# Optimization experiments

Measured on AMD Instinct MI355X. Metric: run time of the kernel, lower is better.

## Reference

```python
import jax, jax.numpy as jnp
import numpy as np

G, N_PER, P_EDGE = 128, 20, 0.2
INPUT_DIM, HIDDEN, OUT_DIM = 32, 64, 10


def _build_structures():
    rng = np.random.default_rng(0)
    n, g = N_PER, G
    A = rng.random((g, n, n)) < P_EDGE
    A = np.triu(A, 1)
    A = A | A.transpose(0, 2, 1)  # symmetric, zero diag
    gi, uu, vv = np.nonzero(A)
    edge_index = np.stack([uu + gi * n, vv + gi * n]).astype(np.int64)
    batch = np.repeat(np.arange(g), n).astype(np.int64)
    # ---- 2-sets ----
    iu, ju = np.triu_indices(n, 1)
    P2 = len(iu)
    M2 = np.zeros((n, n), np.int64)
    M2[iu, ju] = np.arange(P2); M2[ju, iu] = np.arange(P2)
    gu2 = (np.arange(g)[:, None] * n + iu[None]).ravel().astype(np.int64)
    gv2 = (np.arange(g)[:, None] * n + ju[None]).ravel().astype(np.int64)
    iso2 = A[:, iu, ju].astype(np.float32).reshape(-1, 1)
    w = np.arange(n)
    # branch A: (u,v) -> (v,w) if adj[v,w] & w!=u & adj[u,w]; branch B symmetric
    condA = A[:, ju, :] & A[:, iu, :] & (w[None, None, :] != iu[None, :, None])
    condB = A[:, iu, :] & A[:, ju, :] & (w[None, None, :] != ju[None, :, None])
    ga_, ia_, wa_ = np.nonzero(condA)
    gb_, ib_, wb_ = np.nonzero(condB)
    src2 = np.concatenate([ia_ + ga_ * P2, ib_ + gb_ * P2])
    dst2 = np.concatenate([M2[ju[ia_], wa_] + ga_ * P2, M2[iu[ib_], wb_] + gb_ * P2])
    two_edges = np.stack([src2, dst2]).astype(np.int64)
    two_batch = np.repeat(np.arange(g), P2).astype(np.int64)
    # ---- 3-sets ----
    trips = np.array([(a, b, c) for a in range(n) for b in range(a + 1, n) for c in range(b + 1, n)], np.int64)
    a, b, c = trips[:, 0], trips[:, 1], trips[:, 2]
    P3 = len(trips)
    M3 = np.zeros((n, n, n), np.int64)
    M3[a, b, c] = np.arange(P3)
    ga3 = (np.arange(g)[:, None] * n + a[None]).ravel().astype(np.int64)
    gb3 = (np.arange(g)[:, None] * n + b[None]).ravel().astype(np.int64)
    gc3 = (np.arange(g)[:, None] * n + c[None]).ravel().astype(np.int64)
    ec = A[:, a, b].astype(np.int64) + A[:, b, c].astype(np.int64) + A[:, a, c].astype(np.int64)
    iso3 = np.eye(4, dtype=np.float32)[ec.reshape(-1)]
    notin = (w[None] != a[:, None]) & (w[None] != b[:, None]) & (w[None] != c[:, None])  # [P3,n]
    srcs, dsts = [], []
    # branches: replace c (keep a,b), replace b (keep a,c), replace a (keep b,c)
    for k0, k1, nbr in ((a, b, c), (a, c, b), (b, c, a)):
        cond = A[:, nbr, :] & notin[None]
        gg_, ii_, dd_ = np.nonzero(cond)
        tri = np.sort(np.stack([k0[ii_], k1[ii_], dd_], 1), 1)
        srcs.append(ii_ + gg_ * P3)
        dsts.append(M3[tri[:, 0], tri[:, 1], tri[:, 2]] + gg_ * P3)
    three_edges = np.stack([np.concatenate(srcs), np.concatenate(dsts)]).astype(np.int64)
    three_batch = np.repeat(np.arange(g), P3).astype(np.int64)
    x = rng.standard_normal((g * n, INPUT_DIM)).astype(np.float32)
    return (x, edge_index, batch, gu2, gv2, iso2, two_edges, two_batch,
            ga3, gb3, gc3, iso3, three_edges, three_batch)


def setup_inputs() -> dict:
    (x, edge_index, batch, gu2, gv2, iso2, two_edges, two_batch,
     ga3, gb3, gc3, iso3, three_edges, three_batch) = _build_structures()
    rw = np.random.default_rng(1)
    def W(o, i):
        return jnp.asarray((rw.standard_normal((o, i)) * 0.1).astype(np.float32))
    H = HIDDEN
    return dict(
        x=jnp.asarray(x), edge_index=jnp.asarray(edge_index), batch=jnp.asarray(batch),
        gu2=jnp.asarray(gu2), gv2=jnp.asarray(gv2), iso2=jnp.asarray(iso2),
        two_edges=jnp.asarray(two_edges), two_batch=jnp.asarray(two_batch),
        ga3=jnp.asarray(ga3), gb3=jnp.asarray(gb3), gc3=jnp.asarray(gc3),
        iso3=jnp.asarray(iso3), three_edges=jnp.asarray(three_edges),
        three_batch=jnp.asarray(three_batch),
        g1W1_0=W(H, INPUT_DIM), g1W2_0=W(H, INPUT_DIM),
        g1W1_1=W(H, H), g1W2_1=W(H, H), g1W1_2=W(H, H), g1W2_2=W(H, H),
        g2W1_0=W(H, 2 * H + 1), g2W2_0=W(H, 2 * H + 1), g2W1_1=W(H, H), g2W2_1=W(H, H),
        g3W1_0=W(H, 3 * H + 4), g3W2_0=W(H, 3 * H + 4), g3W1_1=W(H, H), g3W2_1=W(H, H),
        cW1=W(H, 3 * H), cb1=jnp.zeros((H,), jnp.float32),
        cW2=W(OUT_DIM, H), cb2=jnp.zeros((OUT_DIM,), jnp.float32),
    )


def _layer(h, W1, W2, src, dst, num):
    # f(s) = relu(h W1^T + scatter_add(h W2^T gathered at src, dst))
    msg = (h @ W2.T)[src]  # project-then-gather; same math as gather-then-project
    nb = jax.ops.segment_sum(msg, dst, num_segments=num)
    return jax.nn.relu(h @ W1.T + nb)


def reference(x, edge_index, batch, gu2, gv2, iso2, two_edges, two_batch,
              ga3, gb3, gc3, iso3, three_edges, three_batch,
              g1W1_0, g1W2_0, g1W1_1, g1W2_1, g1W1_2, g1W2_2,
              g2W1_0, g2W2_0, g2W1_1, g2W2_1,
              g3W1_0, g3W2_0, g3W1_1, g3W2_1,
              cW1, cb1, cW2, cb2):
    N = x.shape[0]
    h = x
    for W1, W2 in ((g1W1_0, g1W2_0), (g1W1_1, g1W2_1), (g1W1_2, g1W2_2)):
        h = _layer(h, W1, W2, edge_index[0], edge_index[1], N)
    emb1 = jax.ops.segment_sum(h, batch, num_segments=G)
    h2 = jnp.concatenate([h[gu2], h[gv2], iso2], axis=1)
    n2 = h2.shape[0]
    for W1, W2 in ((g2W1_0, g2W2_0), (g2W1_1, g2W2_1)):
        h2 = _layer(h2, W1, W2, two_edges[0], two_edges[1], n2)
    emb2 = jax.ops.segment_sum(h2, two_batch, num_segments=G)
    h3 = jnp.concatenate([h[ga3], h[gb3], h[gc3], iso3], axis=1)
    n3 = h3.shape[0]
    for W1, W2 in ((g3W1_0, g3W2_0), (g3W1_1, g3W2_1)):
        h3 = _layer(h3, W1, W2, three_edges[0], three_edges[1], n3)
    emb3 = jax.ops.segment_sum(h3, three_batch, num_segments=G)
    comb = jnp.concatenate([emb1, emb2, emb3], axis=1)
    hid = jax.nn.relu(comb @ cW1.T + cb1)  # dropout is identity in eval mode
    return hid @ cW2.T + cb2
```

## Files before the change

kernel.cpp:

```cpp
#include <hip/hip_runtime.h>
#include <hip/hip_bf16.h>

#define HID 64
#define MROWS 1140
#define PAD1 20
#define PAD2 40
#define PAD3 60

typedef __hip_bfloat16  bf16;
typedef __hip_bfloat162 bf162;
typedef unsigned short  u16;
typedef __attribute__((ext_vector_type(8))) short bf8v;
typedef __attribute__((ext_vector_type(4))) float f4v;
typedef __attribute__((ext_vector_type(4))) unsigned int u4v;
__device__ __forceinline__ float bl(bf16 h) { return __bfloat162float(h); }

__global__ void zero_k(int* p, int n) {
    int i = blockIdx.x * 256 + threadIdx.x;
    if (i < n) p[i] = 0;
}

__global__ void fillp_k(const int* e1, int E1, int* c1, u16* s1, int p1, int P1_,
                        const int* e2, int E2, int* c2, u16* s2, int p2, int P2_,
                        const int* e3, int E3, int* c3, u16* s3, int p3, int P3_,
                        int nb1, int nb2) {
    int b = blockIdx.x;
    const int* edges; int E; int* cur; u16* csrc; int pad; int P; int lb;
    if (b < nb1)            { edges = e1; E = E1; cur = c1; csrc = s1; pad = p1; P = P1_; lb = b; }
    else if (b < nb1 + nb2) { edges = e2; E = E2; cur = c2; csrc = s2; pad = p2; P = P2_; lb = b - nb1; }
    else                    { edges = e3; E = E3; cur = c3; csrc = s3; pad = p3; P = P3_; lb = b - nb1 - nb2; }
    int e = lb * 256 + threadIdx.x;
    if (e >= E) return;
    int d = edges[E + e];
    int slot = atomicAdd(&cur[d], 1);
    if (slot < pad) csrc[(size_t)d * pad + slot] = (u16)(edges[e] % P);
}

__global__ __launch_bounds__(256)
void level1_k(const float* __restrict__ x,
              const int* __restrict__ cnt1, const u16* __restrict__ csrc1,
              const float* __restrict__ W10, const float* __restrict__ W20,
              const float* __restrict__ W11, const float* __restrict__ W21,
              const float* __restrict__ W12, const float* __restrict__ W22,
              float* __restrict__ hout, float* __restrict__ comb, int nper) {
    __shared__ float hbuf[20][64];
    __shared__ float mbuf[20][64];
    __shared__ float wl1[64 * 64];
    __shared__ float wl2[64 * 64];
    int g = blockIdx.x, t = threadIdx.x;
    int wv = t >> 6, lane = t & 63;
    int base = g * nper;
    for (int i = t; i < 20 * 32; i += 256)
        hbuf[i >> 5][i & 31] = x[(size_t)base * 32 + i];
    const float* W1s[3] = {W10, W11, W12};
    const float* W2s[3] = {W20, W21, W22};
#pragma unroll 1
    for (int l = 0; l < 3; ++l) {
        int K = (l == 0) ? 32 : 64;
        const float* W1 = W1s[l];
        const float* W2 = W2s[l];
        __syncthreads();
        for (int i = t; i < K * 64; i += 256) {
            int k = i >> 6, col = i & 63;
            wl1[i] = W1[col * K + k];
            wl2[i] = W2[col * K + k];
        }
        __syncthreads();
        float accz[5], accm[5];
#pragma unroll
        for (int ri = 0; ri < 5; ++ri) {
            int r = wv + ri * 4;
            float az = 0.f, am = 0.f;
            for (int k = 0; k < K; ++k) {
                float hv = hbuf[r][k];
                az = fmaf(hv, wl1[k * 64 + lane], az);
                am = fmaf(hv, wl2[k * 64 + lane], am);
            }
            accz[ri] = az; accm[ri] = am;
        }
        __syncthreads();
#pragma unroll
        for (int ri = 0; ri < 5; ++ri)
            mbuf[wv + ri * 4][lane] = accm[ri];
        __syncthreads();
#pragma unroll
        for (int ri = 0; ri < 5; ++ri) {
            int r = wv + ri * 4;
            float acc = accz[ri];
            int cnt = cnt1[base + r];
            const u16* cs = csrc1 + (size_t)(base + r) * PAD1;
            for (int k = 0; k < cnt; ++k)
                acc += mbuf[cs[k]][lane];
            hbuf[r][lane] = fmaxf(acc, 0.f);
        }
    }
    __syncthreads();
    for (int i = t; i < 20 * 64; i += 256)
        hout[(size_t)base * 64 + i] = hbuf[i >> 6][i & 63];
    if (t < 64) {
        float s = 0.f;
#pragma unroll
        for (int r = 0; r < 20; ++r) s += hbuf[r][t];
        comb[g * 192 + t] = s;
    }
}

struct FJob {
    const float *hsrc;
    const float *W1t, *W2t;
    const int *ga, *gb, *gc;
    const float *iso;
    const float *wc1, *wc2; int ldw, isoC, nT;
    const float *Wl1, *Wl2;
    const u16 *csrc; const int *cnt; int pad;
    bf16 *zc; bf16 *m1g;
    int P, ntiles, comboff;
};

__device__ __forceinline__ int msw(int row, int ch) {
    return (row << 6) + ((ch ^ (row & 7)) << 3);
}
__device__ __forceinline__ void accu4(u4v v, float* f) {
#pragma unroll
    for (int i = 0; i < 4; ++i) {
        f[2 * i]     += __uint_as_float(v[i] << 16);
        f[2 * i + 1] += __uint_as_float(v[i] & 0xffff0000u);
    }
}
__device__ __forceinline__ void accxy4(u4v v, float* zx, float* zy) {
#pragma unroll
    for (int i = 0; i < 4; ++i) {
        zx[i] += __uint_as_float(v[i] << 16);
        zy[i] += __uint_as_float(v[i] & 0xffff0000u);
    }
}
__device__ __forceinline__ bf8v pack8(const float* f) {
    bf16 tmp[8];
#pragma unroll
    for (int e = 0; e < 8; ++e) tmp[e] = __float2bfloat16(f[e]);
    bf8v r; __builtin_memcpy(&r, tmp, 16); return r;
}
__device__ __forceinline__ bf8v pack8relu(const float* f) {
    bf16 tmp[8];
#pragma unroll
    for (int e = 0; e < 8; ++e) tmp[e] = __float2bfloat16(fmaxf(f[e], 0.f));
    bf8v r; __builtin_memcpy(&r, tmp, 16); return r;
}
__device__ __forceinline__ u4v asu4(bf8v v) { u4v r; __builtin_memcpy(&r, &v, 16); return r; }
__device__ __forceinline__ void hsacc(const bf162* tb, int nd, int c4, float* zx, float* zy) {
    u4v v0 = *(const u4v*)(tb + (nd << 6) + (((c4    ) ^ (nd & 15)) << 2));
    u4v v1 = *(const u4v*)(tb + (nd << 6) + (((c4 + 1) ^ (nd & 15)) << 2));
    accxy4(v0, zx, zy);
    accxy4(v1, zx + 4, zy + 4);
}
__device__ __forceinline__ void hsaccY(const bf162* tb, int nd, int c4, float* zy) {
    u4v v0 = *(const u4v*)(tb + (nd << 6) + (((c4    ) ^ (nd & 15)) << 2));
    u4v v1 = *(const u4v*)(tb + (nd << 6) + (((c4 + 1) ^ (nd & 15)) << 2));
#pragma unroll
    for (int i = 0; i < 4; ++i) {
        zy[i]     += __uint_as_float(v0[i] & 0xffff0000u);
        zy[4 + i] += __uint_as_float(v1[i] & 0xffff0000u);
    }
}
__device__ __forceinline__ void naccum(const bf16* mL, int nbr, int quad, float* acc) {
    u4v v0 = *(const u4v*)(mL + msw(nbr, quad));
    u4v v1 = *(const u4v*)(mL + msw(nbr, quad + 4));
    accu4(v0, acc); accu4(v1, acc + 8);
}

__device__ __forceinline__ void run_k1(const FJob& jb, int g, int h,
                                       bf16* mLDS, bf16* wstage) {
    int t = threadIdx.x;
    const int P = jb.P, nT = jb.nT;
    const int gbase = g * P, nb20 = g * 20;
    int lane = t & 63, wv = t >> 6, quad = lane >> 4, m16 = lane & 15;

    bf162* hsA = (bf162*)wstage;
    const bf162* hsB = hsA + 1280;
    const bf162* hsC = hsA + 2560;
    bf16* mW = mLDS;
    for (int i = t; i < nT * 8192; i += 1024) {
        int table = i >> 13, r = i & 8191;
        int e = r & 7, mm = (r >> 3) & 15, qq = (r >> 7) & 3;
        int kk = (r >> 9) & 1, mat = (r >> 10) & 1, nn = r >> 11;
        const float* W = mat ? jb.W2t : jb.W1t;
        mW[i] = __float2bfloat16(W[(size_t)(nn * 16 + mm) * jb.ldw + table * 64 + kk * 32 + qq * 8 + e]);
    }
    float* wcT = (float*)(wstage + 7680);
    if (t < 512) {
        int mat = t >> 8, c = (t >> 6) & 3, f = t & 63;
        const float* W = mat ? jb.wc2 : jb.wc1;
        wcT[mat * 256 + c * 64 + f] = (c < jb.isoC) ? W[f * jb.ldw + c] : 0.f;
    }
    __syncthreads();
    if (wv < nT) {
        const bf16* mWt = mW + wv * 8192;
        bf8v a[2][2];
#pragma unroll
        for (int rt = 0; rt < 2; ++rt) {
            int node = rt * 16 + m16;
#pragma unroll
            for (int kt = 0; kt < 2; ++kt) {
                float tmp[8] = {0.f, 0.f, 0.f, 0.f, 0.f, 0.f, 0.f, 0.f};
                if (node < 20) {
                    const float* hr = jb.hsrc + (size_t)(nb20 + node) * 64 + kt * 32 + quad * 8;
#pragma unroll
                    for (int e = 0; e < 8; ++e) tmp[e] = hr[e];
                }
                a[rt][kt] = pack8(tmp);
            }
        }
        bf162* hsT = hsA + wv * 1280;
#pragma unroll
        for (int n = 0; n < 4; ++n) {
            const bf8v b1k0 = *(const bf8v*)(mWt + ((((n*2+0)*2+0)*4+quad)*16+m16)*8);
            const bf8v b1k1 = *(const bf8v*)(mWt + ((((n*2+0)*2+1)*4+quad)*16+m16)*8);
            const bf8v b2k0 = *(const bf8v*)(mWt + ((((n*2+1)*2+0)*4+quad)*16+m16)*8);
            const bf8v b2k1 = *(const bf8v*)(mWt + ((((n*2+1)*2+1)*4+quad)*16+m16)*8);
#pragma unroll
            for (int rt = 0; rt < 2; ++rt) {
                f4v acca = {0.f, 0.f, 0.f, 0.f};
                f4v accb = {0.f, 0.f, 0.f, 0.f};
                acca = __builtin_amdgcn_mfma_f32_16x16x32_bf16(a[rt][0], b1k0, acca, 0, 0, 0);
                acca = __builtin_amdgcn_mfma_f32_16x16x32_bf16(a[rt][1], b1k1, acca, 0, 0, 0);
                accb = __builtin_amdgcn_mfma_f32_16x16x32_bf16(a[rt][0], b2k0, accb, 0, 0, 0);
                accb = __builtin_amdgcn_mfma_f32_16x16x32_bf16(a[rt][1], b2k1, accb, 0, 0, 0);
                int col = n * 16 + m16, c4 = col >> 2;
#pragma unroll
                for (int r = 0; r < 4; ++r) {
                    int node = rt * 16 + quad * 4 + r;
                    if (node < 20) {
                        bf162 v; v.x = __float2bfloat16(acca[r]); v.y = __float2bfloat16(accb[r]);
                        hsT[(node << 6) + ((c4 ^ (node & 15)) << 2) + (col & 3)] = v;
                    }
                }
            }
        }
    }
    __syncthreads();

    bf8v z8[3][2];
#pragma unroll
    for (int k = 0; k < 3; ++k) {
        int tile = wv + k * 16;
        if (tile >= jb.ntiles) continue;
#pragma unroll
        for (int rt = 0; rt < 2; ++rt) {
            bool own = (rt == h);
            int row = tile * 32 + rt * 16 + m16;
            float zx[16], zy[16];
#pragma unroll
            for (int j = 0; j < 16; ++j) { zx[j] = 0.f; zy[j] = 0.f; }
            if (row < P) {
                size_t gr = (size_t)gbase + row;
                int na = jb.ga[gr] - nb20;
                int nb = jb.gb[gr] - nb20;
                int nc = 0;
                const float* w1r; const float* w2r; float isw;
                if (nT == 3) {
                    nc = jb.gc[gr] - nb20;
                    float4 iv = ((const float4*)jb.iso)[gr];
                    int ec = (int)(iv.y + 2.f * iv.z + 3.f * iv.w + 0.5f);
                    w1r = wcT + ec * 64; w2r = wcT + 256 + ec * 64; isw = 1.f;
                } else {
                    w1r = wcT; w2r = wcT + 256; isw = jb.iso[gr];
                }
#pragma unroll
                for (int kt = 0; kt < 2; ++kt) {
                    int c4 = kt * 8 + quad * 2;
                    int f0 = kt * 32 + quad * 8;
                    if (own) {
                        hsacc(hsA, na, c4, zx + kt * 8, zy + kt * 8);
                        hsacc(hsB, nb, c4, zx + kt * 8, zy + kt * 8);
                        if (nT == 3) hsacc(hsC, nc, c4, zx + kt * 8, zy + kt * 8);
#pragma unroll
                        for (int e = 0; e < 8; ++e)
                            zx[kt * 8 + e] = fmaf(isw, w1r[f0 + e], zx[kt * 8 + e]);
                    } else {
                        hsaccY(hsA, na, c4, zy + kt * 8);
                        hsaccY(hsB, nb, c4, zy + kt * 8);
                        if (nT == 3) hsaccY(hsC, nc, c4, zy + kt * 8);
                    }
#pragma unroll
                    for (int e = 0; e < 8; ++e)
                        zy[kt * 8 + e] = fmaf(isw, w2r[f0 + e], zy[kt * 8 + e]);
                }
                *(bf8v*)(mLDS + msw(row, quad))     = pack8(zy);
                *(bf8v*)(mLDS + msw(row, quad + 4)) = pack8(zy + 8);
            }
            if (own) { z8[k][0] = pack8(zx); z8[k][1] = pack8(zx + 8); }
        }
    }
    __syncthreads();

    for (int i = t; i < 8192; i += 1024) {
        int e = i & 7, mm = (i >> 3) & 15, qq = (i >> 7) & 3;
        int kk = (i >> 9) & 1, mat = (i >> 10) & 1, nn = i >> 11;
        const float* W = mat ? jb.Wl2 : jb.Wl1;
        wstage[i] = __float2bfloat16(W[(nn * 16 + mm) * HID + kk * 32 + qq * 8 + e]);
    }
#pragma unroll
    for (int k = 0; k < 3; ++k) {
        int tile = wv + k * 16;
        if (tile >= jb.ntiles) continue;
        int row = tile * 32 + h * 16 + m16;
        float acc[16];
#pragma unroll
        for (int j = 0; j < 16; ++j) acc[j] = 0.f;
        accu4(asu4(z8[k][0]), acc);
        accu4(asu4(z8[k][1]), acc + 8);
        if (row < P) {
            size_t gr = (size_t)gbase + row;
            int cnt = jb.cnt[gr];
            const u16* cs = jb.csrc + gr * (size_t)jb.pad;
            int kk = 0;
            for (; kk + 4 <= cnt; kk += 4) {
                int n0 = cs[kk], n1 = cs[kk + 1], n2 = cs[kk + 2], n3 = cs[kk + 3];
                naccum(mLDS, n0, quad, acc); naccum(mLDS, n1, quad, acc);
                naccum(mLDS, n2, quad, acc); naccum(mLDS, n3, quad, acc);
            }
            for (; kk < cnt; ++kk) naccum(mLDS, cs[kk], quad, acc);
        }
        z8[k][0] = pack8relu(acc);
        z8[k][1] = pack8relu(acc + 8);
    }
    __syncthreads();

#pragma unroll
    for (int k = 0; k < 3; ++k) {
        int tile = wv + k * 16;
        if (tile >= jb.ntiles) continue;
        int j0 = tile * 32;
#pragma unroll
        for (int n = 0; n < 4; ++n) {
            const bf8v b1k0 = *(const bf8v*)(wstage + ((((n*2+0)*2+0)*4+quad)*16+m16)*8);
            const bf8v b1k1 = *(const bf8v*)(wstage + ((((n*2+0)*2+1)*4+quad)*16+m16)*8);
            const bf8v b2k0 = *(const bf8v*)(wstage + ((((n*2+1)*2+0)*4+quad)*16+m16)*8);
            const bf8v b2k1 = *(const bf8v*)(wstage + ((((n*2+1)*2+1)*4+quad)*16+m16)*8);
            f4v acca = {0.f, 0.f, 0.f, 0.f};
            f4v accb = {0.f, 0.f, 0.f, 0.f};
            acca = __builtin_amdgcn_mfma_f32_16x16x32_bf16(z8[k][0], b1k0, acca, 0, 0, 0);
            acca = __builtin_amdgcn_mfma_f32_16x16x32_bf16(z8[k][1], b1k1, acca, 0, 0, 0);
            accb = __builtin_amdgcn_mfma_f32_16x16x32_bf16(z8[k][0], b2k0, accb, 0, 0, 0);
            accb = __builtin_amdgcn_mfma_f32_16x16x32_bf16(z8[k][1], b2k1, accb, 0, 0, 0);
            int col = n * 16 + m16;
#pragma unroll
            for (int r = 0; r < 4; ++r) {
                int row = j0 + h * 16 + quad * 4 + r;
                if (row < P) {
                    jb.zc[((size_t)gbase + row) * HID + col]  = __float2bfloat16(acca[r]);
                    jb.m1g[((size_t)gbase + row) * HID + col] = __float2bfloat16(accb[r]);
                }
            }
        }
    }
}

__global__ __launch_bounds__(1024, 1)
void fused23a_k(FJob j3, FJob j2, float* __restrict__ comb, int G) {
    __shared__ __align__(16) bf16 mLDS[MROWS * HID];
    __shared__ __align__(16) bf16 wstage[8768];
    int b = blockIdx.x;
    int g = b >> 1, h = b & 1;
    if (h == 0 && threadIdx.x < 128) comb[g * 192 + 64 + threadIdx.x] = 0.f;
    run_k1(j3, g, h, mLDS, wstage);
    __syncthreads();
    run_k1(j2, g, h, mLDS, wstage);
}

__device__ __forceinline__ void run_k2(const FJob& jb, int g, int h,
                                       bf16* mLDS, float* part, float* comb) {
    int t = threadIdx.x;
    const int P = jb.P;
    const int gbase = g * P;
    int lane = t & 63, wv = t >> 6, quad = lane >> 4, m16 = lane & 15;
    for (int i = t; i < P * 8; i += 1024) {
        int row = i >> 3, ch = i & 7;
        u4v v = *(const u4v*)(jb.m1g + ((size_t)gbase + row) * HID + ch * 8);
        *(u4v*)(mLDS + msw(row, ch)) = v;
    }
    __syncthreads();
    float ps[16];
#pragma unroll
    for (int j = 0; j < 16; ++j) ps[j] = 0.f;
#pragma unroll
    for (int k = 0; k < 3; ++k) {
        int tile = wv + k * 16;
        if (tile >= jb.ntiles) continue;
        int row = tile * 32 + h * 16 + m16;
        if (row < P) {
            float acc[16];
#pragma unroll
            for (int j = 0; j < 16; ++j) acc[j] = 0.f;
            size_t gr = (size_t)gbase + row;
            u4v zc0 = *(const u4v*)(jb.zc + gr * HID + quad * 8);
            u4v zc1 = *(const u4v*)(jb.zc + gr * HID + 32 + quad * 8);
            accu4(zc0, acc); accu4(zc1, acc + 8);
            int cnt = jb.cnt[gr];
            const u16* cs = jb.csrc + gr * (size_t)jb.pad;
            int kk = 0;
            for (; kk + 4 <= cnt; kk += 4) {
                int n0 = cs[kk], n1 = cs[kk + 1], n2 = cs[kk + 2], n3 = cs[kk + 3];
                naccum(mLDS, n0, quad, acc); naccum(mLDS, n1, quad, acc);
                naccum(mLDS, n2, quad, acc); naccum(mLDS, n3, quad, acc);
            }
            for (; kk < cnt; ++kk) naccum(mLDS, cs[kk], quad, acc);
#pragma unroll
            for (int j = 0; j < 16; ++j) ps[j] += fmaxf(acc[j], 0.f);
        }
    }
#pragma unroll
    for (int j = 0; j < 16; ++j) {
        ps[j] += __shfl_xor(ps[j], 1, 64);
        ps[j] += __shfl_xor(ps[j], 2, 64);
        ps[j] += __shfl_xor(ps[j], 4, 64);
        ps[j] += __shfl_xor(ps[j], 8, 64);
    }
    if (m16 == 0) {
#pragma unroll
        for (int kt = 0; kt < 2; ++kt)
#pragma unroll
            for (int e = 0; e < 8; ++e)
                part[wv * 64 + kt * 32 + quad * 8 + e] = ps[kt * 8 + e];
    }
    __syncthreads();
    if (t < 64) {
        float s = 0.f;
#pragma unroll
        for (int w = 0; w < 16; ++w) s += part[w * 64 + t];
        atomicAdd(&comb[g * 192 + jb.comboff + t], s);
    }
    __syncthreads();
}

__global__ __launch_bounds__(1024, 1)
void fused23b_k(FJob j3, FJob j2, float* __restrict__ comb, int G) {
    __shared__ __align__(16) bf16 mLDS[MROWS * HID];
    __shared__ float part[1024];
    int b = blockIdx.x;
    int g = b >> 1, h = b & 1;
    run_k2(j3, g, h, mLDS, part, comb);
    run_k2(j2, g, h, mLDS, part, comb);
}

__global__ void classifier_k(const float* __restrict__ comb,
                             const float* __restrict__ cW1, const float* __restrict__ cb1,
                             const float* __restrict__ cW2, const float* __restrict__ cb2,
                             float* __restrict__ out) {
    __shared__ float row[192];
    __shared__ float hid[64];
    int g = blockIdx.x, t = threadIdx.x;
    for (int i = t; i < 192; i += 64) row[i] = comb[g * 192 + i];
    __syncthreads();
    float acc = cb1[t];
#pragma unroll 8
    for (int k = 0; k < 192; ++k) acc += row[k] * cW1[t * 192 + k];
    hid[t] = fmaxf(acc, 0.f);
    __syncthreads();
    if (t < 10) {
        float o = cb2[t];
#pragma unroll
        for (int k = 0; k < 64; ++k) o += hid[k] * cW2[t * 64 + k];
        out[g * 10 + t] = o;
    }
}

static inline int cdiv(long long a, long long b) { return (int)((a + b - 1) / b); }

extern "C" void kernel_launch(void* const* d_in, const int* in_sizes, int n_in,
                              void* d_out, int out_size, void* d_ws, size_t ws_size,
                              hipStream_t stream) {
    const float* x        = (const float*)d_in[0];
    const int*   eidx     = (const int*)d_in[1];
    const int*   gu2      = (const int*)d_in[3];
    const int*   gv2      = (const int*)d_in[4];
    const float* iso2     = (const float*)d_in[5];
    const int*   tedges   = (const int*)d_in[6];
    const int*   ga3      = (const int*)d_in[8];
    const int*   gb3      = (const int*)d_in[9];
    const int*   gc3      = (const int*)d_in[10];
    const float* iso3     = (const float*)d_in[11];
    const int*   hedges   = (const int*)d_in[12];
    const float* g1W1[3]  = {(const float*)d_in[14], (const float*)d_in[16], (const float*)d_in[18]};
    const float* g1W2[3]  = {(const float*)d_in[15], (const float*)d_in[17], (const float*)d_in[19]};
    const float* g2W1_0   = (const float*)d_in[20];
    const float* g2W2_0   = (const float*)d_in[21];
    const float* g2W1_1   = (const float*)d_in[22];
    const float* g2W2_1   = (const float*)d_in[23];
    const float* g3W1_0   = (const float*)d_in[24];
    const float* g3W2_0   = (const float*)d_in[25];
    const float* g3W1_1   = (const float*)d_in[26];
    const float* g3W2_1   = (const float*)d_in[27];
    const float* cW1      = (const float*)d_in[28];
    const float* cb1      = (const float*)d_in[29];
    const float* cW2      = (const float*)d_in[30];
    const float* cb2      = (const float*)d_in[31];
    float* out = (float*)d_out;

    const int N  = in_sizes[0] / 32;
    const int E1 = in_sizes[1] / 2;
    const int n2 = in_sizes[3];
    const int E2 = in_sizes[6] / 2;
    const int n3 = in_sizes[8];
    const int E3 = in_sizes[12] / 2;
    const int G  = out_size / 10;
    const int per1 = N / G, per2 = n2 / G, per3 = n3 / G;

    float* ws = (float*)d_ws;
    size_t off = 0;
    auto alloc = [&](size_t n) { off = (off + 3) & ~(size_t)3; float* p = ws + off; off += n; return p; };
    const size_t NH = (size_t)N * HID;
    float* h0 = alloc(NH);
    bf16* z2c = (bf16*)alloc((size_t)n2 * HID / 2 + 64);
    bf16* z3c = (bf16*)alloc((size_t)n3 * HID / 2 + 64);
    bf16* m2g = (bf16*)alloc((size_t)n2 * HID / 2 + 64);
    bf16* m3g = (bf16*)alloc((size_t)n3 * HID / 2 + 64);
    float* comb = alloc((size_t)G * 192);
    int* iws = (int*)(ws + off);
    size_t ioff = 0;
    auto ialloc = [&](size_t n) { int* p = iws + ioff; ioff += n; return p; };
    int* cur1 = ialloc(N); int* cur2 = ialloc(n2); int* cur3 = ialloc(n3);
    u16* u16ws = (u16*)(iws + ioff);
    size_t uoff = 0;
    auto ualloc = [&](size_t n) { u16* p = u16ws + uoff; uoff += n; return p; };
    u16* csrc1 = ualloc((size_t)N * PAD1);
    u16* csrc2 = ualloc((size_t)n2 * PAD2);
    u16* csrc3 = ualloc((size_t)n3 * PAD3);
    (void)ws_size;

    dim3 B256(256);

    int ncnt = N + n2 + n3;
    zero_k<<<cdiv(ncnt, 256), B256, 0, stream>>>(cur1, ncnt);
    int ne1 = cdiv(E1, 256), ne2 = cdiv(E2, 256), ne3 = cdiv(E3, 256);
    fillp_k<<<ne1 + ne2 + ne3, B256, 0, stream>>>(
        eidx, E1, cur1, csrc1, PAD1, per1,
        tedges, E2, cur2, csrc2, PAD2, per2,
        hedges, E3, cur3, csrc3, PAD3, per3, ne1, ne2);

    level1_k<<<G, B256, 0, stream>>>(x, cur1, csrc1,
        g1W1[0], g1W2[0], g1W1[1], g1W2[1], g1W1[2], g1W2[2], h0, comb, per1);

    {
        FJob j3, j2;
        j3.hsrc = h0; j3.W1t = g3W1_0; j3.W2t = g3W2_0;
        j3.ga = ga3; j3.gb = gb3; j3.gc = gc3;
        j3.iso = iso3; j3.wc1 = g3W1_0 + 192; j3.wc2 = g3W2_0 + 192;
        j3.ldw = 196; j3.isoC = 4; j3.nT = 3;
        j3.Wl1 = g3W1_1; j3.Wl2 = g3W2_1;
        j3.csrc = csrc3; j3.cnt = cur3; j3.pad = PAD3;
        j3.zc = z3c; j3.m1g = m3g;
        j3.P = per3; j3.ntiles = (per3 + 31) >> 5; j3.comboff = 128;

        j2.hsrc = h0; j2.W1t = g2W1_0; j2.W2t = g2W2_0;
        j2.ga = gu2; j2.gb = gv2; j2.gc = nullptr;
        j2.iso = iso2; j2.wc1 = g2W1_0 + 128; j2.wc2 = g2W2_0 + 128;
        j2.ldw = 129; j2.isoC = 1; j2.nT = 2;
        j2.Wl1 = g2W1_1; j2.Wl2 = g2W2_1;
        j2.csrc = csrc2; j2.cnt = cur2; j2.pad = PAD2;
        j2.zc = z2c; j2.m1g = m2g;
        j2.P = per2; j2.ntiles = (per2 + 31) >> 5; j2.comboff = 64;

        fused23a_k<<<2 * G, 1024, 0, stream>>>(j3, j2, comb, G);
        fused23b_k<<<2 * G, 1024, 0, stream>>>(j3, j2, comb, G);
    }

    classifier_k<<<G, 64, 0, stream>>>(comb, cW1, cb1, cW2, cb2, out);
}
```

Before: 269.3 us.

## Fuse level-1 GNN layers into fused23a kernel, keeping node features in LDS

```diff
diff --git a/kernel.cpp b/kernel.cpp
--- a/kernel.cpp
+++ b/kernel.cpp
@@ -36,77 +36,7 @@
     if (slot < pad) csrc[(size_t)d * pad + slot] = (u16)(edges[e] % P);
 }
 
-__global__ __launch_bounds__(256)
-void level1_k(const float* __restrict__ x,
-              const int* __restrict__ cnt1, const u16* __restrict__ csrc1,
-              const float* __restrict__ W10, const float* __restrict__ W20,
-              const float* __restrict__ W11, const float* __restrict__ W21,
-              const float* __restrict__ W12, const float* __restrict__ W22,
-              float* __restrict__ hout, float* __restrict__ comb, int nper) {
-    __shared__ float hbuf[20][64];
-    __shared__ float mbuf[20][64];
-    __shared__ float wl1[64 * 64];
-    __shared__ float wl2[64 * 64];
-    int g = blockIdx.x, t = threadIdx.x;
-    int wv = t >> 6, lane = t & 63;
-    int base = g * nper;
-    for (int i = t; i < 20 * 32; i += 256)
-        hbuf[i >> 5][i & 31] = x[(size_t)base * 32 + i];
-    const float* W1s[3] = {W10, W11, W12};
-    const float* W2s[3] = {W20, W21, W22};
-#pragma unroll 1
-    for (int l = 0; l < 3; ++l) {
-        int K = (l == 0) ? 32 : 64;
-        const float* W1 = W1s[l];
-        const float* W2 = W2s[l];
-        __syncthreads();
-        for (int i = t; i < K * 64; i += 256) {
-            int k = i >> 6, col = i & 63;
-            wl1[i] = W1[col * K + k];
-            wl2[i] = W2[col * K + k];
-        }
-        __syncthreads();
-        float accz[5], accm[5];
-#pragma unroll
-        for (int ri = 0; ri < 5; ++ri) {
-            int r = wv + ri * 4;
-            float az = 0.f, am = 0.f;
-            for (int k = 0; k < K; ++k) {
-                float hv = hbuf[r][k];
-                az = fmaf(hv, wl1[k * 64 + lane], az);
-                am = fmaf(hv, wl2[k * 64 + lane], am);
-            }
-            accz[ri] = az; accm[ri] = am;
-        }
-        __syncthreads();
-#pragma unroll
-        for (int ri = 0; ri < 5; ++ri)
-            mbuf[wv + ri * 4][lane] = accm[ri];
-        __syncthreads();
-#pragma unroll
-        for (int ri = 0; ri < 5; ++ri) {
-            int r = wv + ri * 4;
-            float acc = accz[ri];
-            int cnt = cnt1[base + r];
-            const u16* cs = csrc1 + (size_t)(base + r) * PAD1;
-            for (int k = 0; k < cnt; ++k)
-                acc += mbuf[cs[k]][lane];
-            hbuf[r][lane] = fmaxf(acc, 0.f);
-        }
-    }
-    __syncthreads();
-    for (int i = t; i < 20 * 64; i += 256)
-        hout[(size_t)base * 64 + i] = hbuf[i >> 6][i & 63];
-    if (t < 64) {
-        float s = 0.f;
-#pragma unroll
-        for (int r = 0; r < 20; ++r) s += hbuf[r][t];
-        comb[g * 192 + t] = s;
-    }
-}
-
 struct FJob {
-    const float *hsrc;
     const float *W1t, *W2t;
     const int *ga, *gb, *gc;
     const float *iso;
@@ -169,7 +99,7 @@
 }
 
 __device__ __forceinline__ void run_k1(const FJob& jb, int g, int h,
-                                       bf16* mLDS, bf16* wstage) {
+                                       bf16* mLDS, bf16* wstage, const float* hb) {
     int t = threadIdx.x;
     const int P = jb.P, nT = jb.nT;
     const int gbase = g * P, nb20 = g * 20;
@@ -203,7 +133,7 @@
             for (int kt = 0; kt < 2; ++kt) {
                 float tmp[8] = {0.f, 0.f, 0.f, 0.f, 0.f, 0.f, 0.f, 0.f};
                 if (node < 20) {
-                    const float* hr = jb.hsrc + (size_t)(nb20 + node) * 64 + kt * 32 + quad * 8;
+                    const float* hr = hb + node * 65 + kt * 32 + quad * 8;
 #pragma unroll
                     for (int e = 0; e < 8; ++e) tmp[e] = hr[e];
                 }
@@ -357,15 +287,79 @@
 }
 
 __global__ __launch_bounds__(1024, 1)
-void fused23a_k(FJob j3, FJob j2, float* __restrict__ comb, int G) {
+void fused23a_k(const float* __restrict__ x,
+                const int* __restrict__ cnt1, const u16* __restrict__ csrc1,
+                const float* __restrict__ W10, const float* __restrict__ W20,
+                const float* __restrict__ W11, const float* __restrict__ W21,
+                const float* __restrict__ W12, const float* __restrict__ W22,
+                FJob j3, FJob j2, float* __restrict__ comb, int G) {
     __shared__ __align__(16) bf16 mLDS[MROWS * HID];
     __shared__ __align__(16) bf16 wstage[8768];
-    int b = blockIdx.x;
+    int b = blockIdx.x, t = threadIdx.x;
     int g = b >> 1, h = b & 1;
-    if (h == 0 && threadIdx.x < 128) comb[g * 192 + 64 + threadIdx.x] = 0.f;
-    run_k1(j3, g, h, mLDS, wstage);
-    __syncthreads();
-    run_k1(j2, g, h, mLDS, wstage);
+    if (h == 0 && t < 128) comb[g * 192 + 64 + t] = 0.f;
+
+    float* hb  = (float*)(mLDS + 70360);
+    float* mb  = (float*)(mLDS + 67800);
+    float* wlA = (float*)mLDS;
+    float* wlB = wlA + 64 * 65;
+    int col = t & 63, r0 = t >> 6;
+    bool has2 = r0 < 4; int r1 = 16 + r0;
+    if (t < 640) hb[(t >> 5) * 65 + (t & 31)] = x[(size_t)g * 640 + t];
+    const float* W1s[3] = {W10, W11, W12};
+    const float* W2s[3] = {W20, W21, W22};
+#pragma unroll 1
+    for (int l = 0; l < 3; ++l) {
+        const int K = l ? 64 : 32, LD = K + 1;
+        const float* W1 = W1s[l];
+        const float* W2 = W2s[l];
+        __syncthreads();
+        for (int i = t; i < K * 64; i += 1024) {
+            int c = i / K, k = i - c * K;
+            wlA[c * LD + k] = W1[i];
+            wlB[c * LD + k] = W2[i];
+        }
+        __syncthreads();
+        float az0 = 0.f, am0 = 0.f, az1 = 0.f, am1 = 0.f;
+        const float* wr1 = wlA + col * LD;
+        const float* wr2 = wlB + col * LD;
+        for (int k = 0; k < K; ++k) {
+            float w1v = wr1[k], w2v = wr2[k];
+            float h0v = hb[r0 * 65 + k];
+            az0 = fmaf(h0v, w1v, az0); am0 = fmaf(h0v, w2v, am0);
+            if (has2) {
+                float h1v = hb[r1 * 65 + k];
+                az1 = fmaf(h1v, w1v, az1); am1 = fmaf(h1v, w2v, am1);
+            }
+        }
+        mb[r0 * 64 + col] = am0;
+        if (has2) mb[r1 * 64 + col] = am1;
+        __syncthreads();
+        {
+            int cnt = cnt1[g * 20 + r0];
+            const u16* cs = csrc1 + (size_t)(g * 20 + r0) * PAD1;
+            float acc = az0;
+            for (int k = 0; k < cnt; ++k) acc += mb[cs[k] * 64 + col];
+            hb[r0 * 65 + col] = fmaxf(acc, 0.f);
+        }
+        if (has2) {
+            int cnt = cnt1[g * 20 + r1];
+            const u16* cs = csrc1 + (size_t)(g * 20 + r1) * PAD1;
+            float acc = az1;
+            for (int k = 0; k < cnt; ++k) acc += mb[cs[k] * 64 + col];
+            hb[r1 * 65 + col] = fmaxf(acc, 0.f);
+        }
+    }
+    __syncthreads();
+    if (h == 0 && t < 64) {
+        float s = 0.f;
+#pragma unroll
+        for (int r = 0; r < 20; ++r) s += hb[r * 65 + t];
+        comb[g * 192 + t] = s;
+    }
+    run_k1(j2, g, h, mLDS, wstage, hb);
+    __syncthreads();
+    run_k1(j3, g, h, mLDS, wstage, hb);
 }
 
 __device__ __forceinline__ void run_k2(const FJob& jb, int g, int h,
@@ -509,8 +503,6 @@
     float* ws = (float*)d_ws;
     size_t off = 0;
     auto alloc = [&](size_t n) { off = (off + 3) & ~(size_t)3; float* p = ws + off; off += n; return p; };
-    const size_t NH = (size_t)N * HID;
-    float* h0 = alloc(NH);
     bf16* z2c = (bf16*)alloc((size_t)n2 * HID / 2 + 64);
     bf16* z3c = (bf16*)alloc((size_t)n3 * HID / 2 + 64);
     bf16* m2g = (bf16*)alloc((size_t)n2 * HID / 2 + 64);
@@ -538,12 +530,9 @@
         tedges, E2, cur2, csrc2, PAD2, per2,
         hedges, E3, cur3, csrc3, PAD3, per3, ne1, ne2);
 
-    level1_k<<<G, B256, 0, stream>>>(x, cur1, csrc1,
-        g1W1[0], g1W2[0], g1W1[1], g1W2[1], g1W1[2], g1W2[2], h0, comb, per1);
-
     {
         FJob j3, j2;
-        j3.hsrc = h0; j3.W1t = g3W1_0; j3.W2t = g3W2_0;
+        j3.W1t = g3W1_0; j3.W2t = g3W2_0;
         j3.ga = ga3; j3.gb = gb3; j3.gc = gc3;
         j3.iso = iso3; j3.wc1 = g3W1_0 + 192; j3.wc2 = g3W2_0 + 192;
         j3.ldw = 196; j3.isoC = 4; j3.nT = 3;
@@ -552,7 +541,7 @@
         j3.zc = z3c; j3.m1g = m3g;
         j3.P = per3; j3.ntiles = (per3 + 31) >> 5; j3.comboff = 128;
 
-        j2.hsrc = h0; j2.W1t = g2W1_0; j2.W2t = g2W2_0;
+        j2.W1t = g2W1_0; j2.W2t = g2W2_0;
         j2.ga = gu2; j2.gb = gv2; j2.gc = nullptr;
         j2.iso = iso2; j2.wc1 = g2W1_0 + 128; j2.wc2 = g2W2_0 + 128;
         j2.ldw = 129; j2.isoC = 1; j2.nT = 2;
@@ -561,7 +550,8 @@
         j2.zc = z2c; j2.m1g = m2g;
         j2.P = per2; j2.ntiles = (per2 + 31) >> 5; j2.comboff = 64;
 
-        fused23a_k<<<2 * G, 1024, 0, stream>>>(j3, j2, comb, G);
+        fused23a_k<<<2 * G, 1024, 0, stream>>>(x, cur1, csrc1,
+            g1W1[0], g1W2[0], g1W1[1], g1W2[1], g1W1[2], g1W2[2], j3, j2, comb, G);
         fused23b_k<<<2 * G, 1024, 0, stream>>>(j3, j2, comb, G);
     }
 
```

After: 264.1 us. Within noise of the previous version (-1.9%).
